# Kernel tuning notes

Measured on AMD Instinct MI355X. Metric: run time of the kernel, lower is better.

Reference implementation:

```python
import jax, jax.numpy as jnp
import numpy as np

SCORE_THR = 0.005   # score_thres is None in init -> default 0.005
IOU_THR = 0.5
TOPK = 1024         # fixed pre-NMS candidate cap (JAX needs static shapes)


def setup_inputs() -> dict:
    key = jax.random.key(0)
    # (B, 4+nc, N_anchors): 16 images, 80 classes, 33600 anchors (1280x1280, strides 8/16/32)
    x = jax.random.normal(key, (16, 84, 33600), dtype=jnp.float32)
    return {"x": x}


def _pairwise_iou(b):
    # b: (K, 4) xyxy. Same math as torchvision.ops.box_iou.
    lt = jnp.maximum(b[:, None, :2], b[None, :, :2])   # (K, K, 2)
    rb = jnp.minimum(b[:, None, 2:], b[None, :, 2:])   # (K, K, 2)
    wh = jnp.clip(rb - lt, 0.0)
    inter = wh[..., 0] * wh[..., 1]
    area = (b[:, 2] - b[:, 0]) * (b[:, 3] - b[:, 1])
    union = area[:, None] + area[None, :] - inter
    return inter / jnp.maximum(union, 1e-9)


def _nms_single(boxes, svals, cids):
    # boxes (N,4); svals (N,) with -inf where score <= threshold; cids (N,) int
    top_s, idx = jax.lax.top_k(svals, TOPK)            # score-descending candidates
    b = boxes[idx]                                      # (K, 4)
    c = cids[idx]                                       # (K,)
    valid = top_s > SCORE_THR                           # thresholded-out slots are -inf
    iou = _pairwise_iou(b)                              # (K, K)
    ar = jnp.arange(TOPK)

    def body(i, keep):
        # greedy NMS: box i (if still kept) suppresses lower-scored boxes with IoU > thr
        sup = (iou[i] > IOU_THR) & (ar > i) & keep[i]
        return keep & ~sup

    keep = jax.lax.fori_loop(0, TOPK, body, valid)
    out = jnp.concatenate([b, top_s[:, None], c[:, None].astype(jnp.float32)], axis=1)  # (K, 6)
    out = jnp.where(keep[:, None], out, 0.0)            # padded fixed-size result
    return out, keep


def reference(x):
    xt = jnp.transpose(x, (0, 2, 1))                    # (B, N, 4+nc)
    boxes, scores = xt[..., :4], xt[..., 4:]
    svals = scores.max(-1)                              # (B, N)
    cids = scores.argmax(-1)                            # (B, N)
    svals = jnp.where(svals > SCORE_THR, svals, -jnp.inf)  # score-threshold mask
    out, keep = jax.vmap(_nms_single)(boxes, svals, cids)
    # out: (B, TOPK, 6) zero-padded [xyxy, score, cls]; keep: (B, TOPK) validity mask
    return out, keep
```

## Files before the change

### kernel.cpp

```cpp
#include <hip/hip_runtime.h>
#include <cstdint>
#include <cstddef>

#define NB 16
#define NC 84
#define NA 33600
#define NCLS 80
#define TOPK 1024
#define NBIN 8192
#define CANDCAP 8192
#define SELCAP 2048
#define SCORE_THR 0.005f
#define IOU_THR 0.5f

__device__ __forceinline__ unsigned mono_u32(float f) {
    unsigned u = __float_as_uint(f);
    return (u & 0x80000000u) ? ~u : (u | 0x80000000u);
}
__device__ __forceinline__ float key_val(uint64_t k) {
    unsigned u = (unsigned)(k >> 32);
    u = (u & 0x80000000u) ? (u & 0x7FFFFFFFu) : ~u;
    return __uint_as_float(u);
}
__device__ __forceinline__ int key_idx(uint64_t k) {
    return (int)(~(uint32_t)(k & 0xFFFFFFFFu));
}

__global__ __launch_bounds__(256) void score_kernel(const float* __restrict__ x,
                                                    float* __restrict__ sval,
                                                    int* __restrict__ cid) {
    int gid = blockIdx.x * 256 + threadIdx.x;
    if (gid >= NB * (NA / 4)) return;
    int b = gid / (NA / 4);
    int q = gid - b * (NA / 4);
    const float4* p = (const float4*)(x + (size_t)b * NC * NA + (size_t)4 * NA) + q;
    float4 best = p[0];
    int4 bc = {0, 0, 0, 0};
#pragma unroll 4
    for (int c = 1; c < NCLS; ++c) {
        float4 v = p[(size_t)c * (NA / 4)];
        if (v.x > best.x) { best.x = v.x; bc.x = c; }
        if (v.y > best.y) { best.y = v.y; bc.y = c; }
        if (v.z > best.z) { best.z = v.z; bc.z = c; }
        if (v.w > best.w) { best.w = v.w; bc.w = c; }
    }
    float4 s;
    s.x = (best.x > SCORE_THR) ? best.x : -INFINITY;
    s.y = (best.y > SCORE_THR) ? best.y : -INFINITY;
    s.z = (best.z > SCORE_THR) ? best.z : -INFINITY;
    s.w = (best.w > SCORE_THR) ? best.w : -INFINITY;
    ((float4*)sval)[gid] = s;
    ((int4*)cid)[gid] = bc;
}

__global__ __launch_bounds__(256) void hist_kernel(const float* __restrict__ sval,
                                                   unsigned* __restrict__ hist) {
    int b = blockIdx.x >> 4;
    int sub = blockIdx.x & 15;
    int t = threadIdx.x;
    __shared__ unsigned h[NBIN];
    for (int i = t; i < NBIN; i += 256) h[i] = 0;
    __syncthreads();
    int a0 = sub * (NA / 16), a1 = a0 + (NA / 16);
    const float* sv = sval + (size_t)b * NA;
    for (int a = a0 + t; a < a1; a += 256)
        atomicAdd(&h[mono_u32(sv[a]) >> 19], 1u);
    __syncthreads();
    for (int i = t; i < NBIN; i += 256)
        if (h[i]) atomicAdd(&hist[b * NBIN + i], h[i]);
}

__global__ __launch_bounds__(256) void scan_kernel(const unsigned* __restrict__ hist,
                                                   unsigned* __restrict__ cutbin) {
    int b = blockIdx.x;
    int t = threadIdx.x;
    __shared__ unsigned csum[256];
    const unsigned* h = hist + b * NBIN;
    unsigned local = 0;
#pragma unroll 8
    for (int q = 0; q < 32; ++q) local += h[NBIN - 1 - (t * 32 + q)];
    csum[t] = local;
    __syncthreads();
    for (int off = 1; off < 256; off <<= 1) {
        unsigned v = (t >= off) ? csum[t - off] : 0u;
        __syncthreads();
        csum[t] += v;
        __syncthreads();
    }
    unsigned incl = csum[t], excl = incl - local;
    if (excl < TOPK && incl >= TOPK) {
        unsigned cum = excl;
        for (int q = 0; q < 32; ++q) {
            unsigned bin = NBIN - 1 - (t * 32 + q);
            unsigned c = h[bin];
            if (cum + c >= TOPK) { cutbin[b] = bin; break; }
            cum += c;
        }
    }
}

__global__ __launch_bounds__(256) void compact_kernel(const float* __restrict__ sval,
                                                      const unsigned* __restrict__ cutbin,
                                                      uint64_t* __restrict__ cand,
                                                      unsigned* __restrict__ cnt) {
    int gid = blockIdx.x * 256 + threadIdx.x;
    int b = gid / NA;
    int a = gid - b * NA;
    int b_first = (blockIdx.x * 256) / NA;
    int seg = b - b_first;
    __shared__ unsigned lcnt[2], lbase[2];
    __shared__ uint64_t k0[256], k1[256];
    if (threadIdx.x < 2) lcnt[threadIdx.x] = 0;
    __syncthreads();
    unsigned u = mono_u32(sval[gid]);
    if ((u >> 19) >= cutbin[b]) {
        unsigned pos = atomicAdd(&lcnt[seg], 1u);
        uint64_t key = ((uint64_t)u << 32) | (uint32_t)(~(uint32_t)a);
        if (seg) k1[pos] = key; else k0[pos] = key;
    }
    __syncthreads();
    if (threadIdx.x == 0 && lcnt[0]) lbase[0] = atomicAdd(&cnt[b_first * 64], lcnt[0]);
    if (threadIdx.x == 1 && lcnt[1]) lbase[1] = atomicAdd(&cnt[(b_first + 1) * 64], lcnt[1]);
    __syncthreads();
    if (threadIdx.x < lcnt[0]) {
        unsigned p = lbase[0] + threadIdx.x;
        if (p < CANDCAP) cand[((size_t)b_first << 13) + p] = k0[threadIdx.x];
    }
    if (threadIdx.x < lcnt[1]) {
        unsigned p = lbase[1] + threadIdx.x;
        if (p < CANDCAP) cand[((size_t)(b_first + 1) << 13) + p] = k1[threadIdx.x];
    }
}

__device__ __forceinline__ void bitonic_desc(uint64_t* A, int n, int tid) {
    for (int k = 2; k <= n; k <<= 1) {
        for (int j = k >> 1; j > 0; j >>= 1) {
            for (int i = tid; i < n; i += 256) {
                int ixj = i ^ j;
                if (ixj > i) {
                    uint64_t a = A[i], b2 = A[ixj];
                    bool up = ((i & k) == 0);
                    if (up ? (a < b2) : (a > b2)) { A[i] = b2; A[ixj] = a; }
                }
            }
            __syncthreads();
        }
    }
}

__global__ __launch_bounds__(256) void sortk_kernel(const uint64_t* __restrict__ cand,
                                                    const unsigned* __restrict__ cnt,
                                                    const unsigned* __restrict__ cutbin,
                                                    float* __restrict__ topval,
                                                    int* __restrict__ topidx) {
    int b = blockIdx.x;
    int t = threadIdx.x;
    __shared__ uint64_t lk[CANDCAP];
    __shared__ uint64_t lsel[SELCAP];
    __shared__ unsigned sh[256];
    __shared__ unsigned snA, snSel, ssubcut;
    unsigned C = cnt[b * 64];
    if (C > CANDCAP) C = CANDCAP;
    unsigned cb = cutbin[b];

    for (int i = t; i < CANDCAP; i += 256)
        lk[i] = (i < (int)C) ? cand[((size_t)b << 13) + i] : 0ULL;
    for (int i = t; i < SELCAP; i += 256) lsel[i] = 0ULL;
    for (int i = t; i < 256; i += 256) sh[i] = 0;
    if (t == 0) { snA = 0; snSel = 0; }
    __syncthreads();

    unsigned myA = 0;
    for (int i = t; i < (int)C; i += 256) {
        unsigned u = (unsigned)(lk[i] >> 32);
        if ((u >> 19) > cb) myA++;
        else atomicAdd(&sh[(u >> 11) & 255u], 1u);
    }
    atomicAdd(&snA, myA);
    __syncthreads();

    if (t == 0) {
        unsigned r = TOPK - snA;
        unsigned cum = 0, sc = 0;
        for (int s = 255; s >= 0; --s) {
            cum += sh[s];
            if (cum >= r) { sc = (unsigned)s; break; }
        }
        ssubcut = sc;
    }
    __syncthreads();
    unsigned subcut = ssubcut;

    int lane = t & 63;
    for (int i = t; i < CANDCAP; i += 256) {
        unsigned u = (unsigned)(lk[i] >> 32);
        unsigned bin = u >> 19;
        bool sel = (bin > cb) || (bin == cb && ((u >> 11) & 255u) >= subcut);
        uint64_t mask = __ballot(sel);
        if (mask) {
            int ldr = __ffsll((unsigned long long)mask) - 1;
            unsigned base = 0;
            if (lane == ldr) base = atomicAdd(&snSel, (unsigned)__popcll(mask));
            base = __shfl(base, ldr, 64);
            if (sel) {
                unsigned p = base + (unsigned)__popcll(mask & ((1ULL << lane) - 1ULL));
                if (p < SELCAP) lsel[p] = lk[i];
            }
        }
    }
    __syncthreads();
    unsigned nSel = snSel;

    uint64_t* buf;
    if (nSel <= SELCAP) { bitonic_desc(lsel, SELCAP, t); buf = lsel; }
    else                { bitonic_desc(lk, CANDCAP, t);  buf = lk;  }

    for (int i = t; i < TOPK; i += 256) {
        uint64_t key = buf[i];
        topval[b * TOPK + i] = key_val(key);
        topidx[b * TOPK + i] = key_idx(key);
    }
}

__global__ __launch_bounds__(256) void boxes_kernel(const float* __restrict__ x,
                                                    const int* __restrict__ cid,
                                                    const int* __restrict__ tidx,
                                                    float* __restrict__ bx1, float* __restrict__ by1,
                                                    float* __restrict__ bx2, float* __restrict__ by2,
                                                    float* __restrict__ bar, int* __restrict__ tcid) {
    int b = blockIdx.x;
    int base = b << 10;
    const float* xb = x + (size_t)b * NC * NA;
    for (int k = threadIdx.x; k < TOPK; k += 256) {
        int idx = tidx[base + k];
        float x1 = xb[idx], y1 = xb[NA + idx], x2 = xb[2 * NA + idx], y2 = xb[3 * NA + idx];
        bx1[base + k] = x1; by1[base + k] = y1;
        bx2[base + k] = x2; by2[base + k] = y2;
        bar[base + k] = (x2 - x1) * (y2 - y1);
        tcid[base + k] = cid[b * NA + idx];
    }
}

#define LDSPAD(j) ((j) + ((j) >> 6))
__global__ __launch_bounds__(256) void maskbuild_kernel(const float* __restrict__ bx1,
                                                        const float* __restrict__ by1,
                                                        const float* __restrict__ bx2,
                                                        const float* __restrict__ by2,
                                                        const float* __restrict__ bar,
                                                        const float* __restrict__ tval,
                                                        uint64_t* __restrict__ M,
                                                        int* __restrict__ rowflag) {
    int b = blockIdx.x >> 6;
    int r0 = (blockIdx.x & 63) << 4;
    int t = threadIdx.x;
    int r = r0 + (t >> 4);
    int w = t & 15;
    int base = b << 10;
    __shared__ float sx1[TOPK + 16], sy1[TOPK + 16], sx2[TOPK + 16], sy2[TOPK + 16], sar[TOPK + 16];
    __shared__ int anyf[256];

    for (int j = t; j < TOPK; j += 256) {
        int ji = LDSPAD(j);
        sx1[ji] = bx1[base + j]; sy1[ji] = by1[base + j];
        sx2[ji] = bx2[base + j]; sy2[ji] = by2[base + j];
        sar[ji] = bar[base + j];
    }
    __syncthreads();

    int ri = LDSPAD(r);
    float ix1 = sx1[ri], iy1 = sy1[ri], ix2 = sx2[ri], iy2 = sy2[ri], ia = sar[ri];
    uint64_t m = 0;
#pragma unroll 8
    for (int jj = 0; jj < 64; ++jj) {
        int j = (w << 6) + jj;
        int ji = w * 65 + jj;
        float ltx = fmaxf(ix1, sx1[ji]);
        float lty = fmaxf(iy1, sy1[ji]);
        float rbx = fminf(ix2, sx2[ji]);
        float rby = fminf(iy2, sy2[ji]);
        float ww = fmaxf(rbx - ltx, 0.0f);
        float hh = fmaxf(rby - lty, 0.0f);
        float inter = ww * hh;
        float uni = ia + sar[ji] - inter;
        float iou = inter / fmaxf(uni, 1e-9f);
        if (j > r && iou > IOU_THR) m |= (1ULL << jj);
    }
    M[((size_t)(base + r) << 4) + w] = m;
    anyf[t] = (m != 0ULL);
    __syncthreads();
    if (w == 0) {
        int any = 0;
#pragma unroll
        for (int q = 0; q < 16; ++q) any |= anyf[t + q];
        bool valid = tval[base + r] > SCORE_THR;
        rowflag[base + r] = (any && valid) ? 1 : 0;
    }
}

__global__ __launch_bounds__(64) void sweep_kernel(const uint64_t* __restrict__ M,
                                                   const int* __restrict__ rowflag,
                                                   const float* __restrict__ tval,
                                                   const int* __restrict__ tcid,
                                                   const float* __restrict__ bx1,
                                                   const float* __restrict__ by1,
                                                   const float* __restrict__ bx2,
                                                   const float* __restrict__ by2,
                                                   float* __restrict__ out) {
    int b = blockIdx.x;
    int l = threadIdx.x;
    int base = b << 10;
    int w = l & 15, g = l >> 4;
    __shared__ int list[TOPK];

    float tv[16];
#pragma unroll
    for (int s = 0; s < 16; ++s) tv[s] = tval[base + (s << 6) + l];

    uint64_t vword = 0;
#pragma unroll
    for (int s = 0; s < 16; ++s) {
        uint64_t bal = __ballot(tv[s] > SCORE_THR);
        if (l == s) vword = bal;
    }

    int cnt = 0;
#pragma unroll
    for (int s = 0; s < 16; ++s) {
        int flag = rowflag[base + (s << 6) + l];
        uint64_t m = __ballot(flag != 0);
        if (flag) {
            int pos = cnt + __popcll(m & ((1ULL << l) - 1ULL));
            list[pos] = (s << 6) + l;
        }
        cnt += __popcll(m);
    }
    __syncthreads();

    uint64_t remv = 0;
    for (int chunk = 0; chunk < cnt; chunk += 64) {
        int m = min(64, cnt - chunk);
        int idx_l = chunk + l;
        int myi = list[(idx_l < cnt) ? idx_l : 0];
        uint64_t rows[16];
#pragma unroll
        for (int q = 0; q < 16; ++q) {
            int it = chunk + q * 4 + g;
            int it2 = (it < cnt) ? it : 0;
            uint64_t v = M[((size_t)(base + list[it2]) << 4) + w];
            rows[q] = (it < cnt) ? v : 0ULL;
        }
        for (int r = 0; r < m; ++r) {
            int i = __shfl(myi, r, 64);
            uint64_t row = __shfl(rows[r >> 2], ((r & 3) << 4) + w, 64);
            uint64_t rb = __shfl(remv, i >> 6, 64);
            bool kept = !((rb >> (i & 63)) & 1ULL);
            remv |= (kept && l < 16) ? row : 0ULL;
        }
    }

    uint64_t kf = vword & ~remv;
#pragma unroll
    for (int s = 0; s < 16; ++s) {
        uint64_t kw = __shfl(kf, s, 64);
        bool kp = (kw >> l) & 1ULL;
        int k = (s << 6) + l;
        float x1 = bx1[base + k], y1 = by1[base + k];
        float x2 = bx2[base + k], y2 = by2[base + k];
        float* po = out + ((size_t)(base + k)) * 6;
        po[0] = kp ? x1 : 0.0f;
        po[1] = kp ? y1 : 0.0f;
        po[2] = kp ? x2 : 0.0f;
        po[3] = kp ? y2 : 0.0f;
        po[4] = kp ? tv[s] : 0.0f;
        po[5] = kp ? (float)tcid[base + k] : 0.0f;
        out[(size_t)NB * TOPK * 6 + base + k] = kp ? 1.0f : 0.0f;
    }
}

extern "C" void kernel_launch(void* const* d_in, const int* in_sizes, int n_in,
                              void* d_out, int out_size, void* d_ws, size_t ws_size,
                              hipStream_t stream) {
    const float* x = (const float*)d_in[0];
    float* out = (float*)d_out;
    char* ws = (char*)d_ws;

    size_t off = 0;
    auto alloc = [&](size_t bytes) { void* p = ws + off; off = (off + bytes + 255) & ~(size_t)255; return p; };
    float*    sval    = (float*)alloc((size_t)NB * NA * 4);
    int*      cid     = (int*)alloc((size_t)NB * NA * 4);
    unsigned* hist    = (unsigned*)alloc((size_t)NB * NBIN * 4);
    unsigned* cutbin  = (unsigned*)alloc(NB * 4);
    unsigned* cnt     = (unsigned*)alloc((size_t)NB * 64 * 4);
    uint64_t* cand    = (uint64_t*)alloc((size_t)NB * CANDCAP * 8);
    float*    tval    = (float*)alloc((size_t)NB * TOPK * 4);
    int*      tidx    = (int*)alloc((size_t)NB * TOPK * 4);
    float*    bx1     = (float*)alloc((size_t)NB * TOPK * 4);
    float*    by1     = (float*)alloc((size_t)NB * TOPK * 4);
    float*    bx2     = (float*)alloc((size_t)NB * TOPK * 4);
    float*    by2     = (float*)alloc((size_t)NB * TOPK * 4);
    float*    bar     = (float*)alloc((size_t)NB * TOPK * 4);
    int*      tcid    = (int*)alloc((size_t)NB * TOPK * 4);
    int*      rowflag = (int*)alloc((size_t)NB * TOPK * 4);
    uint64_t* M       = (uint64_t*)alloc((size_t)NB * TOPK * 16 * 8);

    hipMemsetAsync(hist, 0, (size_t)NB * NBIN * 4, stream);
    hipMemsetAsync(cnt, 0, (size_t)NB * 64 * 4, stream);

    score_kernel<<<NB * (NA / 4) / 256, 256, 0, stream>>>(x, sval, cid);
    hist_kernel<<<NB * 16, 256, 0, stream>>>(sval, hist);
    scan_kernel<<<NB, 256, 0, stream>>>(hist, cutbin);
    compact_kernel<<<NB * NA / 256, 256, 0, stream>>>(sval, cutbin, cand, cnt);
    sortk_kernel<<<NB, 256, 0, stream>>>(cand, cnt, cutbin, tval, tidx);
    boxes_kernel<<<NB, 256, 0, stream>>>(x, cid, tidx, bx1, by1, bx2, by2, bar, tcid);
    maskbuild_kernel<<<NB * 64, 256, 0, stream>>>(bx1, by1, bx2, by2, bar, tval, M, rowflag);
    sweep_kernel<<<NB, 64, 0, stream>>>(M, rowflag, tval, tcid, bx1, by1, bx2, by2, out);
}
```

Measured before the change: 412.5 us.

## Fuse post-score NMS stages into one persistent kernel with grid barriers

Replaces the hist/scan/compact/sortk/boxes/maskbuild/sweep launches with a single 128-block persistent kernel that uses atomic spin grid barriers between phases. The score kernel now zeroes the barrier counters and candidate counts, which removes the memsets. The histogram moves to one block per image. The aim is to cut the launch overhead and inter-kernel gaps of many small kernels. The cost is lower parallelism in the histogram and mask stages, and a reliance on all 128 blocks being co-resident for the barrier to be safe.

```diff
diff --git a/kernel.cpp b/kernel.cpp
--- a/kernel.cpp
+++ b/kernel.cpp
@@ -12,6 +12,7 @@
 #define SELCAP 2048
 #define SCORE_THR 0.005f
 #define IOU_THR 0.5f
+#define MEGA_NBLK 128
 
 __device__ __forceinline__ unsigned mono_u32(float f) {
     unsigned u = __float_as_uint(f);
@@ -28,7 +29,13 @@
 
 __global__ __launch_bounds__(256) void score_kernel(const float* __restrict__ x,
                                                     float* __restrict__ sval,
-                                                    int* __restrict__ cid) {
+                                                    int* __restrict__ cid,
+                                                    unsigned* __restrict__ bar,
+                                                    unsigned* __restrict__ cnt) {
+    if (blockIdx.x == 0) {
+        if (threadIdx.x < 8) bar[threadIdx.x] = 0;
+        cnt[threadIdx.x] = 0;
+    }
     int gid = blockIdx.x * 256 + threadIdx.x;
     if (gid >= NB * (NA / 4)) return;
     int b = gid / (NA / 4);
@@ -36,7 +43,7 @@
     const float4* p = (const float4*)(x + (size_t)b * NC * NA + (size_t)4 * NA) + q;
     float4 best = p[0];
     int4 bc = {0, 0, 0, 0};
-#pragma unroll 4
+#pragma unroll 8
     for (int c = 1; c < NCLS; ++c) {
         float4 v = p[(size_t)c * (NA / 4)];
         if (v.x > best.x) { best.x = v.x; bc.x = c; }
@@ -53,83 +60,17 @@
     ((int4*)cid)[gid] = bc;
 }
 
-__global__ __launch_bounds__(256) void hist_kernel(const float* __restrict__ sval,
-                                                   unsigned* __restrict__ hist) {
-    int b = blockIdx.x >> 4;
-    int sub = blockIdx.x & 15;
-    int t = threadIdx.x;
-    __shared__ unsigned h[NBIN];
-    for (int i = t; i < NBIN; i += 256) h[i] = 0;
+__device__ __forceinline__ void grid_barrier(unsigned* bar, int id) {
     __syncthreads();
-    int a0 = sub * (NA / 16), a1 = a0 + (NA / 16);
-    const float* sv = sval + (size_t)b * NA;
-    for (int a = a0 + t; a < a1; a += 256)
-        atomicAdd(&h[mono_u32(sv[a]) >> 19], 1u);
+    __threadfence();
+    if (threadIdx.x == 0) {
+        __hip_atomic_fetch_add(&bar[id], 1u, __ATOMIC_ACQ_REL, __HIP_MEMORY_SCOPE_AGENT);
+        while (__hip_atomic_load(&bar[id], __ATOMIC_ACQUIRE, __HIP_MEMORY_SCOPE_AGENT)
+               < (unsigned)MEGA_NBLK)
+            __builtin_amdgcn_s_sleep(8);
+    }
     __syncthreads();
-    for (int i = t; i < NBIN; i += 256)
-        if (h[i]) atomicAdd(&hist[b * NBIN + i], h[i]);
-}
-
-__global__ __launch_bounds__(256) void scan_kernel(const unsigned* __restrict__ hist,
-                                                   unsigned* __restrict__ cutbin) {
-    int b = blockIdx.x;
-    int t = threadIdx.x;
-    __shared__ unsigned csum[256];
-    const unsigned* h = hist + b * NBIN;
-    unsigned local = 0;
-#pragma unroll 8
-    for (int q = 0; q < 32; ++q) local += h[NBIN - 1 - (t * 32 + q)];
-    csum[t] = local;
-    __syncthreads();
-    for (int off = 1; off < 256; off <<= 1) {
-        unsigned v = (t >= off) ? csum[t - off] : 0u;
-        __syncthreads();
-        csum[t] += v;
-        __syncthreads();
-    }
-    unsigned incl = csum[t], excl = incl - local;
-    if (excl < TOPK && incl >= TOPK) {
-        unsigned cum = excl;
-        for (int q = 0; q < 32; ++q) {
-            unsigned bin = NBIN - 1 - (t * 32 + q);
-            unsigned c = h[bin];
-            if (cum + c >= TOPK) { cutbin[b] = bin; break; }
-            cum += c;
-        }
-    }
-}
-
-__global__ __launch_bounds__(256) void compact_kernel(const float* __restrict__ sval,
-                                                      const unsigned* __restrict__ cutbin,
-                                                      uint64_t* __restrict__ cand,
-                                                      unsigned* __restrict__ cnt) {
-    int gid = blockIdx.x * 256 + threadIdx.x;
-    int b = gid / NA;
-    int a = gid - b * NA;
-    int b_first = (blockIdx.x * 256) / NA;
-    int seg = b - b_first;
-    __shared__ unsigned lcnt[2], lbase[2];
-    __shared__ uint64_t k0[256], k1[256];
-    if (threadIdx.x < 2) lcnt[threadIdx.x] = 0;
-    __syncthreads();
-    unsigned u = mono_u32(sval[gid]);
-    if ((u >> 19) >= cutbin[b]) {
-        unsigned pos = atomicAdd(&lcnt[seg], 1u);
-        uint64_t key = ((uint64_t)u << 32) | (uint32_t)(~(uint32_t)a);
-        if (seg) k1[pos] = key; else k0[pos] = key;
-    }
-    __syncthreads();
-    if (threadIdx.x == 0 && lcnt[0]) lbase[0] = atomicAdd(&cnt[b_first * 64], lcnt[0]);
-    if (threadIdx.x == 1 && lcnt[1]) lbase[1] = atomicAdd(&cnt[(b_first + 1) * 64], lcnt[1]);
-    __syncthreads();
-    if (threadIdx.x < lcnt[0]) {
-        unsigned p = lbase[0] + threadIdx.x;
-        if (p < CANDCAP) cand[((size_t)b_first << 13) + p] = k0[threadIdx.x];
-    }
-    if (threadIdx.x < lcnt[1]) {
-        unsigned p = lbase[1] + threadIdx.x;
-        if (p < CANDCAP) cand[((size_t)(b_first + 1) << 13) + p] = k1[threadIdx.x];
-    }
+    __threadfence();
 }
 
 __device__ __forceinline__ void bitonic_desc(uint64_t* A, int n, int tid) {
@@ -148,232 +89,280 @@
     }
 }
 
-__global__ __launch_bounds__(256) void sortk_kernel(const uint64_t* __restrict__ cand,
-                                                    const unsigned* __restrict__ cnt,
-                                                    const unsigned* __restrict__ cutbin,
-                                                    float* __restrict__ topval,
-                                                    int* __restrict__ topidx) {
-    int b = blockIdx.x;
-    int t = threadIdx.x;
-    __shared__ uint64_t lk[CANDCAP];
-    __shared__ uint64_t lsel[SELCAP];
-    __shared__ unsigned sh[256];
-    __shared__ unsigned snA, snSel, ssubcut;
-    unsigned C = cnt[b * 64];
-    if (C > CANDCAP) C = CANDCAP;
-    unsigned cb = cutbin[b];
-
-    for (int i = t; i < CANDCAP; i += 256)
-        lk[i] = (i < (int)C) ? cand[((size_t)b << 13) + i] : 0ULL;
-    for (int i = t; i < SELCAP; i += 256) lsel[i] = 0ULL;
-    for (int i = t; i < 256; i += 256) sh[i] = 0;
-    if (t == 0) { snA = 0; snSel = 0; }
-    __syncthreads();
-
-    unsigned myA = 0;
-    for (int i = t; i < (int)C; i += 256) {
-        unsigned u = (unsigned)(lk[i] >> 32);
-        if ((u >> 19) > cb) myA++;
-        else atomicAdd(&sh[(u >> 11) & 255u], 1u);
-    }
-    atomicAdd(&snA, myA);
-    __syncthreads();
-
-    if (t == 0) {
-        unsigned r = TOPK - snA;
-        unsigned cum = 0, sc = 0;
-        for (int s = 255; s >= 0; --s) {
-            cum += sh[s];
-            if (cum >= r) { sc = (unsigned)s; break; }
-        }
-        ssubcut = sc;
-    }
-    __syncthreads();
-    unsigned subcut = ssubcut;
-
-    int lane = t & 63;
-    for (int i = t; i < CANDCAP; i += 256) {
-        unsigned u = (unsigned)(lk[i] >> 32);
-        unsigned bin = u >> 19;
-        bool sel = (bin > cb) || (bin == cb && ((u >> 11) & 255u) >= subcut);
-        uint64_t mask = __ballot(sel);
-        if (mask) {
-            int ldr = __ffsll((unsigned long long)mask) - 1;
-            unsigned base = 0;
-            if (lane == ldr) base = atomicAdd(&snSel, (unsigned)__popcll(mask));
-            base = __shfl(base, ldr, 64);
-            if (sel) {
-                unsigned p = base + (unsigned)__popcll(mask & ((1ULL << lane) - 1ULL));
-                if (p < SELCAP) lsel[p] = lk[i];
-            }
-        }
-    }
-    __syncthreads();
-    unsigned nSel = snSel;
-
-    uint64_t* buf;
-    if (nSel <= SELCAP) { bitonic_desc(lsel, SELCAP, t); buf = lsel; }
-    else                { bitonic_desc(lk, CANDCAP, t);  buf = lk;  }
-
-    for (int i = t; i < TOPK; i += 256) {
-        uint64_t key = buf[i];
-        topval[b * TOPK + i] = key_val(key);
-        topidx[b * TOPK + i] = key_idx(key);
-    }
-}
-
-__global__ __launch_bounds__(256) void boxes_kernel(const float* __restrict__ x,
-                                                    const int* __restrict__ cid,
-                                                    const int* __restrict__ tidx,
-                                                    float* __restrict__ bx1, float* __restrict__ by1,
-                                                    float* __restrict__ bx2, float* __restrict__ by2,
-                                                    float* __restrict__ bar, int* __restrict__ tcid) {
-    int b = blockIdx.x;
-    int base = b << 10;
-    const float* xb = x + (size_t)b * NC * NA;
-    for (int k = threadIdx.x; k < TOPK; k += 256) {
-        int idx = tidx[base + k];
-        float x1 = xb[idx], y1 = xb[NA + idx], x2 = xb[2 * NA + idx], y2 = xb[3 * NA + idx];
-        bx1[base + k] = x1; by1[base + k] = y1;
-        bx2[base + k] = x2; by2[base + k] = y2;
-        bar[base + k] = (x2 - x1) * (y2 - y1);
-        tcid[base + k] = cid[b * NA + idx];
-    }
-}
-
 #define LDSPAD(j) ((j) + ((j) >> 6))
-__global__ __launch_bounds__(256) void maskbuild_kernel(const float* __restrict__ bx1,
-                                                        const float* __restrict__ by1,
-                                                        const float* __restrict__ bx2,
-                                                        const float* __restrict__ by2,
-                                                        const float* __restrict__ bar,
-                                                        const float* __restrict__ tval,
-                                                        uint64_t* __restrict__ M,
-                                                        int* __restrict__ rowflag) {
-    int b = blockIdx.x >> 6;
-    int r0 = (blockIdx.x & 63) << 4;
-    int t = threadIdx.x;
-    int r = r0 + (t >> 4);
-    int w = t & 15;
-    int base = b << 10;
-    __shared__ float sx1[TOPK + 16], sy1[TOPK + 16], sx2[TOPK + 16], sy2[TOPK + 16], sar[TOPK + 16];
+
+__global__ __launch_bounds__(256) void mega_kernel(const float* __restrict__ x,
+                                                   const float* __restrict__ sval,
+                                                   const int* __restrict__ cid,
+                                                   unsigned* __restrict__ bar,
+                                                   unsigned* __restrict__ cnt,
+                                                   unsigned* __restrict__ cutbin,
+                                                   uint64_t* __restrict__ cand,
+                                                   float* __restrict__ tval,
+                                                   float* __restrict__ bx1, float* __restrict__ by1,
+                                                   float* __restrict__ bx2, float* __restrict__ by2,
+                                                   float* __restrict__ barr, int* __restrict__ tcid,
+                                                   uint64_t* __restrict__ M,
+                                                   int* __restrict__ rowflag,
+                                                   float* __restrict__ out) {
+    __shared__ __align__(16) char smem[81920];
+    __shared__ unsigned csum[256], sh[256];
     __shared__ int anyf[256];
-
-    for (int j = t; j < TOPK; j += 256) {
-        int ji = LDSPAD(j);
-        sx1[ji] = bx1[base + j]; sy1[ji] = by1[base + j];
-        sx2[ji] = bx2[base + j]; sy2[ji] = by2[base + j];
-        sar[ji] = bar[base + j];
-    }
-    __syncthreads();
-
-    int ri = LDSPAD(r);
-    float ix1 = sx1[ri], iy1 = sy1[ri], ix2 = sx2[ri], iy2 = sy2[ri], ia = sar[ri];
-    uint64_t m = 0;
+    __shared__ unsigned snA, snSel, ssubcut, lc, lbase;
+    const int t = threadIdx.x;
+    const int g = blockIdx.x;
+
+    if (g < NB) {
+        unsigned* h = (unsigned*)smem;
+        for (int i = t; i < NBIN; i += 256) h[i] = 0;
+        __syncthreads();
+        const float4* sv4 = (const float4*)(sval + (size_t)g * NA);
+        for (int i = t; i < NA / 4; i += 256) {
+            float4 v = sv4[i];
+            atomicAdd(&h[mono_u32(v.x) >> 19], 1u);
+            atomicAdd(&h[mono_u32(v.y) >> 19], 1u);
+            atomicAdd(&h[mono_u32(v.z) >> 19], 1u);
+            atomicAdd(&h[mono_u32(v.w) >> 19], 1u);
+        }
+        __syncthreads();
+        unsigned local = 0;
 #pragma unroll 8
-    for (int jj = 0; jj < 64; ++jj) {
-        int j = (w << 6) + jj;
-        int ji = w * 65 + jj;
-        float ltx = fmaxf(ix1, sx1[ji]);
-        float lty = fmaxf(iy1, sy1[ji]);
-        float rbx = fminf(ix2, sx2[ji]);
-        float rby = fminf(iy2, sy2[ji]);
-        float ww = fmaxf(rbx - ltx, 0.0f);
-        float hh = fmaxf(rby - lty, 0.0f);
-        float inter = ww * hh;
-        float uni = ia + sar[ji] - inter;
-        float iou = inter / fmaxf(uni, 1e-9f);
-        if (j > r && iou > IOU_THR) m |= (1ULL << jj);
-    }
-    M[((size_t)(base + r) << 4) + w] = m;
-    anyf[t] = (m != 0ULL);
-    __syncthreads();
-    if (w == 0) {
-        int any = 0;
-#pragma unroll
-        for (int q = 0; q < 16; ++q) any |= anyf[t + q];
-        bool valid = tval[base + r] > SCORE_THR;
-        rowflag[base + r] = (any && valid) ? 1 : 0;
-    }
-}
-
-__global__ __launch_bounds__(64) void sweep_kernel(const uint64_t* __restrict__ M,
-                                                   const int* __restrict__ rowflag,
-                                                   const float* __restrict__ tval,
-                                                   const int* __restrict__ tcid,
-                                                   const float* __restrict__ bx1,
-                                                   const float* __restrict__ by1,
-                                                   const float* __restrict__ bx2,
-                                                   const float* __restrict__ by2,
-                                                   float* __restrict__ out) {
-    int b = blockIdx.x;
-    int l = threadIdx.x;
-    int base = b << 10;
-    int w = l & 15, g = l >> 4;
-    __shared__ int list[TOPK];
-
-    float tv[16];
-#pragma unroll
-    for (int s = 0; s < 16; ++s) tv[s] = tval[base + (s << 6) + l];
-
-    uint64_t vword = 0;
-#pragma unroll
-    for (int s = 0; s < 16; ++s) {
-        uint64_t bal = __ballot(tv[s] > SCORE_THR);
-        if (l == s) vword = bal;
-    }
-
-    int cnt = 0;
-#pragma unroll
-    for (int s = 0; s < 16; ++s) {
-        int flag = rowflag[base + (s << 6) + l];
-        uint64_t m = __ballot(flag != 0);
-        if (flag) {
-            int pos = cnt + __popcll(m & ((1ULL << l) - 1ULL));
-            list[pos] = (s << 6) + l;
-        }
-        cnt += __popcll(m);
-    }
-    __syncthreads();
-
-    uint64_t remv = 0;
-    for (int chunk = 0; chunk < cnt; chunk += 64) {
-        int m = min(64, cnt - chunk);
-        int idx_l = chunk + l;
-        int myi = list[(idx_l < cnt) ? idx_l : 0];
-        uint64_t rows[16];
-#pragma unroll
-        for (int q = 0; q < 16; ++q) {
-            int it = chunk + q * 4 + g;
-            int it2 = (it < cnt) ? it : 0;
-            uint64_t v = M[((size_t)(base + list[it2]) << 4) + w];
-            rows[q] = (it < cnt) ? v : 0ULL;
-        }
-        for (int r = 0; r < m; ++r) {
-            int i = __shfl(myi, r, 64);
-            uint64_t row = __shfl(rows[r >> 2], ((r & 3) << 4) + w, 64);
-            uint64_t rb = __shfl(remv, i >> 6, 64);
-            bool kept = !((rb >> (i & 63)) & 1ULL);
-            remv |= (kept && l < 16) ? row : 0ULL;
-        }
-    }
-
-    uint64_t kf = vword & ~remv;
-#pragma unroll
-    for (int s = 0; s < 16; ++s) {
-        uint64_t kw = __shfl(kf, s, 64);
-        bool kp = (kw >> l) & 1ULL;
-        int k = (s << 6) + l;
-        float x1 = bx1[base + k], y1 = by1[base + k];
-        float x2 = bx2[base + k], y2 = by2[base + k];
-        float* po = out + ((size_t)(base + k)) * 6;
-        po[0] = kp ? x1 : 0.0f;
-        po[1] = kp ? y1 : 0.0f;
-        po[2] = kp ? x2 : 0.0f;
-        po[3] = kp ? y2 : 0.0f;
-        po[4] = kp ? tv[s] : 0.0f;
-        po[5] = kp ? (float)tcid[base + k] : 0.0f;
-        out[(size_t)NB * TOPK * 6 + base + k] = kp ? 1.0f : 0.0f;
+        for (int q = 0; q < 32; ++q) local += h[NBIN - 1 - (t * 32 + q)];
+        csum[t] = local;
+        __syncthreads();
+        for (int off = 1; off < 256; off <<= 1) {
+            unsigned v = (t >= off) ? csum[t - off] : 0u;
+            __syncthreads();
+            csum[t] += v;
+            __syncthreads();
+        }
+        unsigned incl = csum[t], excl = incl - local;
+        if (excl < TOPK && incl >= TOPK) {
+            unsigned cum = excl;
+            for (int q = 0; q < 32; ++q) {
+                unsigned bin = NBIN - 1 - (t * 32 + q);
+                unsigned c = h[bin];
+                if (cum + c >= TOPK) { cutbin[g] = bin; break; }
+                cum += c;
+            }
+        }
+    }
+    grid_barrier(bar, 0);
+
+    {
+        int b = g >> 3, s8 = g & 7;
+        int a0 = s8 * (NA / 8), a1 = a0 + (NA / 8);
+        uint64_t* cbuf = (uint64_t*)smem;
+        if (t == 0) lc = 0;
+        __syncthreads();
+        unsigned cb = cutbin[b];
+        const float* sv = sval + (size_t)b * NA;
+        for (int a = a0 + t; a < a1; a += 256) {
+            unsigned u = mono_u32(sv[a]);
+            if ((u >> 19) >= cb) {
+                unsigned pos = atomicAdd(&lc, 1u);
+                cbuf[pos] = ((uint64_t)u << 32) | (uint32_t)(~(uint32_t)a);
+            }
+        }
+        __syncthreads();
+        if (t == 0) lbase = lc ? atomicAdd(&cnt[b * 16], lc) : 0u;
+        __syncthreads();
+        for (unsigned i = t; i < lc; i += 256) {
+            unsigned p = lbase + i;
+            if (p < CANDCAP) cand[((size_t)b << 13) + p] = cbuf[i];
+        }
+    }
+    grid_barrier(bar, 1);
+
+    if (g < NB) {
+        const int b = g;
+        uint64_t* lk   = (uint64_t*)smem;
+        uint64_t* lsel = (uint64_t*)(smem + 65536);
+        unsigned C = cnt[b * 16];
+        if (C > CANDCAP) C = CANDCAP;
+        unsigned cb = cutbin[b];
+        for (int i = t; i < CANDCAP; i += 256)
+            lk[i] = (i < (int)C) ? cand[((size_t)b << 13) + i] : 0ULL;
+        for (int i = t; i < SELCAP; i += 256) lsel[i] = 0ULL;
+        sh[t] = 0;
+        if (t == 0) { snA = 0; snSel = 0; }
+        __syncthreads();
+
+        unsigned myA = 0;
+        for (int i = t; i < (int)C; i += 256) {
+            unsigned u = (unsigned)(lk[i] >> 32);
+            if ((u >> 19) > cb) myA++;
+            else atomicAdd(&sh[(u >> 11) & 255u], 1u);
+        }
+        atomicAdd(&snA, myA);
+        __syncthreads();
+        if (t == 0) {
+            unsigned r = TOPK - snA, cum = 0, sc = 0;
+            for (int s = 255; s >= 0; --s) {
+                cum += sh[s];
+                if (cum >= r) { sc = (unsigned)s; break; }
+            }
+            ssubcut = sc;
+        }
+        __syncthreads();
+        unsigned subcut = ssubcut;
+
+        int lane = t & 63;
+        for (int i = t; i < CANDCAP; i += 256) {
+            unsigned u = (unsigned)(lk[i] >> 32);
+            unsigned bin = u >> 19;
+            bool sel = (bin > cb) || (bin == cb && ((u >> 11) & 255u) >= subcut);
+            uint64_t mask = __ballot(sel);
+            if (mask) {
+                int ldr = __ffsll((unsigned long long)mask) - 1;
+                unsigned base2 = 0;
+                if (lane == ldr) base2 = atomicAdd(&snSel, (unsigned)__popcll(mask));
+                base2 = __shfl(base2, ldr, 64);
+                if (sel) {
+                    unsigned p = base2 + (unsigned)__popcll(mask & ((1ULL << lane) - 1ULL));
+                    if (p < SELCAP) lsel[p] = lk[i];
+                }
+            }
+        }
+        __syncthreads();
+        uint64_t* buf;
+        if (snSel <= SELCAP) { bitonic_desc(lsel, SELCAP, t); buf = lsel; }
+        else                 { bitonic_desc(lk, CANDCAP, t);  buf = lk;  }
+
+        int base = b << 10;
+        const float* xb = x + (size_t)b * NC * NA;
+        for (int k = t; k < TOPK; k += 256) {
+            uint64_t key = buf[k];
+            int idx = key_idx(key);
+            tval[base + k] = key_val(key);
+            float x1 = xb[idx], y1 = xb[NA + idx], x2 = xb[2 * NA + idx], y2 = xb[3 * NA + idx];
+            bx1[base + k] = x1; by1[base + k] = y1;
+            bx2[base + k] = x2; by2[base + k] = y2;
+            barr[base + k] = (x2 - x1) * (y2 - y1);
+            tcid[base + k] = cid[b * NA + idx];
+        }
+    }
+    grid_barrier(bar, 2);
+
+    {
+        int b = g >> 3;
+        int base = b << 10;
+        float* sx1 = (float*)smem;
+        float* sy1 = sx1 + (TOPK + 16);
+        float* sx2 = sy1 + (TOPK + 16);
+        float* sy2 = sx2 + (TOPK + 16);
+        float* sar = sy2 + (TOPK + 16);
+        for (int j = t; j < TOPK; j += 256) {
+            int ji = LDSPAD(j);
+            sx1[ji] = bx1[base + j]; sy1[ji] = by1[base + j];
+            sx2[ji] = bx2[base + j]; sy2[ji] = by2[base + j];
+            sar[ji] = barr[base + j];
+        }
+        __syncthreads();
+        int w = t & 15;
+        for (int pass = 0; pass < 8; ++pass) {
+            int r = (g & 7) * 128 + pass * 16 + (t >> 4);
+            int ri = LDSPAD(r);
+            float ix1 = sx1[ri], iy1 = sy1[ri], ix2 = sx2[ri], iy2 = sy2[ri], ia = sar[ri];
+            uint64_t m = 0;
+#pragma unroll 8
+            for (int jj = 0; jj < 64; ++jj) {
+                int j = (w << 6) + jj;
+                int ji = w * 65 + jj;
+                float ltx = fmaxf(ix1, sx1[ji]);
+                float lty = fmaxf(iy1, sy1[ji]);
+                float rbx = fminf(ix2, sx2[ji]);
+                float rby = fminf(iy2, sy2[ji]);
+                float ww = fmaxf(rbx - ltx, 0.0f);
+                float hh = fmaxf(rby - lty, 0.0f);
+                float inter = ww * hh;
+                float uni = ia + sar[ji] - inter;
+                float iou = inter / fmaxf(uni, 1e-9f);
+                if (j > r && iou > IOU_THR) m |= (1ULL << jj);
+            }
+            M[(((size_t)(base + r)) << 4) + w] = m;
+            anyf[t] = (m != 0ULL);
+            __syncthreads();
+            if (w == 0) {
+                int any = 0;
+#pragma unroll
+                for (int q = 0; q < 16; ++q) any |= anyf[(t & ~15) + q];
+                bool valid = tval[base + r] > SCORE_THR;
+                rowflag[base + r] = (any && valid) ? 1 : 0;
+            }
+            __syncthreads();
+        }
+    }
+    grid_barrier(bar, 3);
+
+    if (g < NB && t < 64) {
+        int b = g, l = t;
+        int base = b << 10;
+        int w = l & 15, gg = l >> 4;
+        int* list = (int*)smem;
+
+        float tv[16];
+#pragma unroll
+        for (int s = 0; s < 16; ++s) tv[s] = tval[base + (s << 6) + l];
+
+        uint64_t vword = 0;
+#pragma unroll
+        for (int s = 0; s < 16; ++s) {
+            uint64_t bal = __ballot(tv[s] > SCORE_THR);
+            if (l == s) vword = bal;
+        }
+
+        int cnt2 = 0;
+#pragma unroll
+        for (int s = 0; s < 16; ++s) {
+            int flag = rowflag[base + (s << 6) + l];
+            uint64_t m = __ballot(flag != 0);
+            if (flag) {
+                int pos = cnt2 + __popcll(m & ((1ULL << l) - 1ULL));
+                list[pos] = (s << 6) + l;
+            }
+            cnt2 += __popcll(m);
+        }
+
+        uint64_t remv = 0;
+        for (int chunk = 0; chunk < cnt2; chunk += 64) {
+            int m = min(64, cnt2 - chunk);
+            int idx_l = chunk + l;
+            int myi = list[(idx_l < cnt2) ? idx_l : 0];
+            uint64_t rows[16];
+#pragma unroll
+            for (int q = 0; q < 16; ++q) {
+                int it = chunk + q * 4 + gg;
+                int it2 = (it < cnt2) ? it : 0;
+                uint64_t v = M[(((size_t)(base + list[it2])) << 4) + w];
+                rows[q] = (it < cnt2) ? v : 0ULL;
+            }
+            for (int r = 0; r < m; ++r) {
+                int i = __shfl(myi, r, 64);
+                uint64_t row = __shfl(rows[r >> 2], ((r & 3) << 4) + w, 64);
+                uint64_t rb = __shfl(remv, i >> 6, 64);
+                bool kept = !((rb >> (i & 63)) & 1ULL);
+                remv |= (kept && l < 16) ? row : 0ULL;
+            }
+        }
+
+        uint64_t kf = vword & ~remv;
+#pragma unroll
+        for (int s = 0; s < 16; ++s) {
+            uint64_t kw = __shfl(kf, s, 64);
+            bool kp = (kw >> l) & 1ULL;
+            int k = (s << 6) + l;
+            float x1 = bx1[base + k], y1 = by1[base + k];
+            float x2 = bx2[base + k], y2 = by2[base + k];
+            float* po = out + ((size_t)(base + k)) * 6;
+            po[0] = kp ? x1 : 0.0f;
+            po[1] = kp ? y1 : 0.0f;
+            po[2] = kp ? x2 : 0.0f;
+            po[3] = kp ? y2 : 0.0f;
+            po[4] = kp ? tv[s] : 0.0f;
+            po[5] = kp ? (float)tcid[base + k] : 0.0f;
+            out[(size_t)NB * TOPK * 6 + base + k] = kp ? 1.0f : 0.0f;
+        }
     }
 }
 
@@ -388,30 +377,22 @@
     auto alloc = [&](size_t bytes) { void* p = ws + off; off = (off + bytes + 255) & ~(size_t)255; return p; };
     float*    sval    = (float*)alloc((size_t)NB * NA * 4);
     int*      cid     = (int*)alloc((size_t)NB * NA * 4);
-    unsigned* hist    = (unsigned*)alloc((size_t)NB * NBIN * 4);
+    unsigned* bar     = (unsigned*)alloc(8 * 4);
+    unsigned* cnt     = (unsigned*)alloc((size_t)NB * 16 * 4);
     unsigned* cutbin  = (unsigned*)alloc(NB * 4);
-    unsigned* cnt     = (unsigned*)alloc((size_t)NB * 64 * 4);
     uint64_t* cand    = (uint64_t*)alloc((size_t)NB * CANDCAP * 8);
     float*    tval    = (float*)alloc((size_t)NB * TOPK * 4);
-    int*      tidx    = (int*)alloc((size_t)NB * TOPK * 4);
     float*    bx1     = (float*)alloc((size_t)NB * TOPK * 4);
     float*    by1     = (float*)alloc((size_t)NB * TOPK * 4);
     float*    bx2     = (float*)alloc((size_t)NB * TOPK * 4);
     float*    by2     = (float*)alloc((size_t)NB * TOPK * 4);
-    float*    bar     = (float*)alloc((size_t)NB * TOPK * 4);
+    float*    barr    = (float*)alloc((size_t)NB * TOPK * 4);
     int*      tcid    = (int*)alloc((size_t)NB * TOPK * 4);
     int*      rowflag = (int*)alloc((size_t)NB * TOPK * 4);
     uint64_t* M       = (uint64_t*)alloc((size_t)NB * TOPK * 16 * 8);
 
-    hipMemsetAsync(hist, 0, (size_t)NB * NBIN * 4, stream);
-    hipMemsetAsync(cnt, 0, (size_t)NB * 64 * 4, stream);
-
-    score_kernel<<<NB * (NA / 4) / 256, 256, 0, stream>>>(x, sval, cid);
-    hist_kernel<<<NB * 16, 256, 0, stream>>>(sval, hist);
-    scan_kernel<<<NB, 256, 0, stream>>>(hist, cutbin);
-    compact_kernel<<<NB * NA / 256, 256, 0, stream>>>(sval, cutbin, cand, cnt);
-    sortk_kernel<<<NB, 256, 0, stream>>>(cand, cnt, cutbin, tval, tidx);
-    boxes_kernel<<<NB, 256, 0, stream>>>(x, cid, tidx, bx1, by1, bx2, by2, bar, tcid);
-    maskbuild_kernel<<<NB * 64, 256, 0, stream>>>(bx1, by1, bx2, by2, bar, tval, M, rowflag);
-    sweep_kernel<<<NB, 64, 0, stream>>>(M, rowflag, tval, tcid, bx1, by1, bx2, by2, out);
-}
+    score_kernel<<<NB * (NA / 4) / 256, 256, 0, stream>>>(x, sval, cid, bar, cnt);
+    mega_kernel<<<MEGA_NBLK, 256, 0, stream>>>(x, sval, cid, bar, cnt, cutbin, cand,
+                                               tval, bx1, by1, bx2, by2, barr, tcid,
+                                               M, rowflag, out);
+}
```

After: 543.8 us. 31.8% more time.
